# Kernel optimization log

Measured on AMD Instinct MI355X. Metric: run time of the kernel, lower is better.

The kernel has to match this reference:

```python
import jax, jax.numpy as jnp
import numpy as np

STRIDE = 1
MAX_STRIDE = 250  # 25 * 10 default


def setup_inputs() -> dict:
    key = jax.random.key(0)
    k1, k2 = jax.random.split(key)
    T = 1_000_000
    prediction = jax.random.normal(k1, (T,), dtype=jnp.float32)
    ground_truth = jax.random.normal(k2, (T,), dtype=jnp.float32)
    return {"prediction": prediction, "ground_truth": ground_truth}


def reference(prediction, ground_truth):
    T = prediction.shape[0]
    lags = jnp.arange(0, MAX_STRIDE, STRIDE)
    idx = jnp.arange(T)

    # ground-truth statistics are lag-independent
    mean_gt = jnp.mean(ground_truth)
    var_gt = jnp.var(ground_truth, ddof=1)  # torch.var is unbiased
    v_gt = ground_truth - mean_gt

    def ccc_at_lag(n):
        # shifted pred: n leading zeros followed by prediction[:-n]
        src = idx - n
        pred = jnp.where(src >= 0, prediction[jnp.clip(src, 0)], 0.0)
        mean_pred = jnp.mean(pred)
        var_pred = jnp.var(pred, ddof=1)
        cov = jnp.mean((pred - mean_pred) * v_gt)  # population covariance
        denom = var_gt + var_pred + (mean_gt - mean_pred) ** 2
        return 2.0 * cov / denom

    cccs = jax.vmap(ccc_at_lag)(lags)  # [n_lags]
    return 1.0 - jnp.mean(cccs)
```

## Files before the change

### kernel.cpp

```cpp
#include <hip/hip_runtime.h>
#include <hip/hip_bf16.h>


#define TC 4096
#define NTHR 512
#define NLAG 256
#define NUSED 250
#define NREP 16
#define GT4 (TC / 4 + 66)
#define STATREP_OFF (NREP * NLAG)
#define COUNTER_OFF (STATREP_OFF + NREP * 16)

__device__ __forceinline__ float4 ld_gt_sw(const float* s_gt, int i4) {
    int s = i4 ^ ((i4 >> 3) & 7);
    return *(const float4*)&s_gt[4 * s];
}

__device__ __forceinline__ float ld_atomic(const float* p) {
    return __hip_atomic_load(p, __ATOMIC_RELAXED, __HIP_MEMORY_SCOPE_AGENT);
}

__global__ __launch_bounds__(NTHR) void ccc_fused(const float* __restrict__ pred,
                                                  const float* __restrict__ gt,
                                                  float* __restrict__ ws,
                                                  float* __restrict__ out,
                                                  int T, int nch) {
    __shared__ __align__(16) float s_pred[TC];
    __shared__ __align__(16) float s_gt[GT4 * 4];
    __shared__ __align__(16) float s_acc[16][NLAG];
    __shared__ float s_red[8][4];
    __shared__ float s_stats[4];
    __shared__ float s_sp64[64];
    __shared__ unsigned s_last;

    const int tid = threadIdx.x;
    const int c = blockIdx.x;
    const int j0 = c * TC;

    float sp = 0.f, qp = 0.f, sg = 0.f, qg = 0.f;
    #pragma unroll 2
    for (int i4 = tid; i4 < TC / 4; i4 += NTHR) {
        int g = j0 + 4 * i4;
        float4 v = make_float4(0.f, 0.f, 0.f, 0.f);
        if (g + 3 < T) v = *(const float4*)&pred[g];
        *(float4*)&s_pred[4 * i4] = v;
        sp += v.x + v.y + v.z + v.w;
        qp += v.x * v.x + v.y * v.y + v.z * v.z + v.w * v.w;
    }
    #pragma unroll 2
    for (int i4 = tid; i4 < GT4; i4 += NTHR) {
        int g = j0 + 4 * i4;
        float4 v = make_float4(0.f, 0.f, 0.f, 0.f);
        if (g + 3 < T) v = *(const float4*)&gt[g];
        int s = i4 ^ ((i4 >> 3) & 7);
        *(float4*)&s_gt[4 * s] = v;
        if (i4 < TC / 4) {
            sg += v.x + v.y + v.z + v.w;
            qg += v.x * v.x + v.y * v.y + v.z * v.z + v.w * v.w;
        }
    }
    __syncthreads();

    const int sub = tid >> 5;
    const int l = tid & 31;
    int gi = sub * 64 + 2 * l;
    const int pi0 = sub * 64;

    float w[12];
    {
        float4 a = ld_gt_sw(s_gt, gi);
        float4 b = ld_gt_sw(s_gt, gi + 1);
        float4 d = ld_gt_sw(s_gt, gi + 2);
        w[0] = a.x; w[1] = a.y; w[2] = a.z; w[3] = a.w;
        w[4] = b.x; w[5] = b.y; w[6] = b.z; w[7] = b.w;
        w[8] = d.x; w[9] = d.y; w[10] = d.z; w[11] = d.w;
    }
    float acc[8] = {0.f, 0.f, 0.f, 0.f, 0.f, 0.f, 0.f, 0.f};

    #pragma unroll 8
    for (int it = 0; it < 64; ++it) {
        float4 nw = ld_gt_sw(s_gt, gi + 3 + it);
        float4 p = *(const float4*)&s_pred[4 * (pi0 + it)];
        #pragma unroll
        for (int k = 0; k < 8; ++k) {
            acc[k] = fmaf(p.x, w[k], acc[k]);
            acc[k] = fmaf(p.y, w[k + 1], acc[k]);
            acc[k] = fmaf(p.z, w[k + 2], acc[k]);
            acc[k] = fmaf(p.w, w[k + 3], acc[k]);
        }
        #pragma unroll
        for (int i = 0; i < 8; ++i) w[i] = w[i + 4];
        w[8] = nw.x; w[9] = nw.y; w[10] = nw.z; w[11] = nw.w;
    }

    const int wv = tid >> 6, ln = tid & 63;
    #pragma unroll
    for (int off = 32; off > 0; off >>= 1) {
        sp += __shfl_down(sp, off, 64);
        qp += __shfl_down(qp, off, 64);
        sg += __shfl_down(sg, off, 64);
        qg += __shfl_down(qg, off, 64);
    }
    if (ln == 0) { s_red[wv][0] = sp; s_red[wv][1] = qp; s_red[wv][2] = sg; s_red[wv][3] = qg; }

    #pragma unroll
    for (int k = 0; k < 8; ++k) s_acc[sub][8 * l + k] = acc[k];
    __syncthreads();

    const int rep = c & (NREP - 1);
    if (tid < NLAG) {
        float lagsum = 0.f;
        #pragma unroll
        for (int s = 0; s < 16; ++s) lagsum += s_acc[s][tid];
        atomicAdd(&ws[rep * NLAG + tid], lagsum);
    }
    if (tid < 4) {
        float v = 0.f;
        #pragma unroll
        for (int w8 = 0; w8 < 8; ++w8) v += s_red[w8][tid];
        atomicAdd(&ws[STATREP_OFF + rep * 16 + tid], v);
    }

    __syncthreads();
    if (tid == 0) {
        unsigned* cnt = (unsigned*)(ws + COUNTER_OFF);
        unsigned old = __hip_atomic_fetch_add(cnt, 1u, __ATOMIC_RELAXED,
                                              __HIP_MEMORY_SCOPE_AGENT);
        unsigned want_poison = 0xAAAAAAAAu + (unsigned)(nch - 1);
        unsigned want_zero = (unsigned)(nch - 1);
        s_last = (old == want_poison || old == want_zero) ? 1u : 0u;
    }
    __syncthreads();
    if (!s_last) return;

    {
        const int lag = tid & 255, h = tid >> 8;
        float a = 0.f;
        #pragma unroll
        for (int r = 8 * h; r < 8 * h + 8; ++r) a += ld_atomic(&ws[r * NLAG + lag]);
        s_acc[h][lag] = a;
    }
    if (tid < 64) s_sp64[tid] = ld_atomic(&ws[STATREP_OFF + (tid >> 2) * 16 + (tid & 3)]);
    if (tid < NLAG) {
        float x = pred[T - NLAG + tid];
        s_pred[tid] = x;
        s_acc[2][tid] = x;
        s_acc[4][tid] = x * x;
    }
    __syncthreads();

    if (tid < 4) {
        float s = 0.f;
        #pragma unroll
        for (int r = 0; r < 16; ++r) s += s_sp64[4 * r + tid];
        s_stats[tid] = s;
    }

    float *sa = s_acc[2], *sb = s_acc[3], *qa = s_acc[4], *qb = s_acc[5];
    for (int d = 1; d < NLAG; d <<= 1) {
        __syncthreads();
        if (tid < NLAG) {
            sb[tid] = sa[tid] + ((tid + d < NLAG) ? sa[tid + d] : 0.f);
            qb[tid] = qa[tid] + ((tid + d < NLAG) ? qa[tid + d] : 0.f);
        }
        float* tmp = sa; sa = sb; sb = tmp;
        tmp = qa; qa = qb; qb = tmp;
    }
    __syncthreads();

    if (tid < NLAG) {
        float lagC = s_acc[0][tid] + s_acc[1][tid];
        float v = 0.f;
        if (tid < NUSED) {
            const float Tf = (float)T;
            float sum_pred = s_stats[0], sumsq_pred = s_stats[1];
            float sum_gt = s_stats[2], sumsq_gt = s_stats[3];
            float mean_gt = sum_gt / Tf;
            float var_gt = (sumsq_gt - sum_gt * sum_gt / Tf) / (Tf - 1.f);
            float tail_s = (tid == 0) ? 0.f : sa[NLAG - tid];
            float tail_q = (tid == 0) ? 0.f : qa[NLAG - tid];
            float S = sum_pred - tail_s;
            float Q = sumsq_pred - tail_q;
            float mean_p = S / Tf;
            float var_p = (Q - S * S / Tf) / (Tf - 1.f);
            float cov = (lagC - mean_gt * S) / Tf;
            float dm = mean_gt - mean_p;
            v = 2.f * cov / (var_gt + var_p + dm * dm);
        }
        s_acc[6][tid] = v;
    }
    __syncthreads();
    for (int s = 128; s > 0; s >>= 1) {
        if (tid < s) s_acc[6][tid] += s_acc[6][tid + s];
        __syncthreads();
    }
    if (tid == 0) out[0] = 1.f - s_acc[6][0] / (float)NUSED;
}

extern "C" void kernel_launch(void* const* d_in, const int* in_sizes, int n_in,
                              void* d_out, int out_size, void* d_ws, size_t ws_size,
                              hipStream_t stream) {
    const float* pred = (const float*)d_in[0];
    const float* gt   = (const float*)d_in[1];
    float* out = (float*)d_out;
    float* ws  = (float*)d_ws;
    const int T = in_sizes[0];
    const int nch = (T + TC - 1) / TC;

    ccc_fused<<<nch, NTHR, 0, stream>>>(pred, gt, ws, out, T, nch);
}
```

Measured before the change: 71.24 us.

## Use packed float2 FMAs for lag correlation and hoist bounds checks

```diff
diff --git a/kernel.cpp b/kernel.cpp
--- a/kernel.cpp
+++ b/kernel.cpp
@@ -10,6 +10,8 @@
 #define GT4 (TC / 4 + 66)
 #define STATREP_OFF (NREP * NLAG)
 #define COUNTER_OFF (STATREP_OFF + NREP * 16)
+
+typedef float f2 __attribute__((ext_vector_type(2)));
 
 __device__ __forceinline__ float4 ld_gt_sw(const float* s_gt, int i4) {
     int s = i4 ^ ((i4 >> 3) & 7);
@@ -38,25 +40,45 @@
     const int j0 = c * TC;
 
     float sp = 0.f, qp = 0.f, sg = 0.f, qg = 0.f;
-    #pragma unroll 2
-    for (int i4 = tid; i4 < TC / 4; i4 += NTHR) {
-        int g = j0 + 4 * i4;
-        float4 v = make_float4(0.f, 0.f, 0.f, 0.f);
-        if (g + 3 < T) v = *(const float4*)&pred[g];
-        *(float4*)&s_pred[4 * i4] = v;
-        sp += v.x + v.y + v.z + v.w;
-        qp += v.x * v.x + v.y * v.y + v.z * v.z + v.w * v.w;
-    }
-    #pragma unroll 2
-    for (int i4 = tid; i4 < GT4; i4 += NTHR) {
-        int g = j0 + 4 * i4;
-        float4 v = make_float4(0.f, 0.f, 0.f, 0.f);
-        if (g + 3 < T) v = *(const float4*)&gt[g];
-        int s = i4 ^ ((i4 >> 3) & 7);
-        *(float4*)&s_gt[4 * s] = v;
-        if (i4 < TC / 4) {
-            sg += v.x + v.y + v.z + v.w;
-            qg += v.x * v.x + v.y * v.y + v.z * v.z + v.w * v.w;
+    if (j0 + 4 * GT4 <= T) {
+        #pragma unroll 2
+        for (int i4 = tid; i4 < TC / 4; i4 += NTHR) {
+            float4 v = *(const float4*)&pred[j0 + 4 * i4];
+            *(float4*)&s_pred[4 * i4] = v;
+            sp += v.x + v.y + v.z + v.w;
+            qp += v.x * v.x + v.y * v.y + v.z * v.z + v.w * v.w;
+        }
+        #pragma unroll 2
+        for (int i4 = tid; i4 < GT4; i4 += NTHR) {
+            float4 v = *(const float4*)&gt[j0 + 4 * i4];
+            int s = i4 ^ ((i4 >> 3) & 7);
+            *(float4*)&s_gt[4 * s] = v;
+            if (i4 < TC / 4) {
+                sg += v.x + v.y + v.z + v.w;
+                qg += v.x * v.x + v.y * v.y + v.z * v.z + v.w * v.w;
+            }
+        }
+    } else {
+        #pragma unroll 2
+        for (int i4 = tid; i4 < TC / 4; i4 += NTHR) {
+            int g = j0 + 4 * i4;
+            float4 v = make_float4(0.f, 0.f, 0.f, 0.f);
+            if (g + 3 < T) v = *(const float4*)&pred[g];
+            *(float4*)&s_pred[4 * i4] = v;
+            sp += v.x + v.y + v.z + v.w;
+            qp += v.x * v.x + v.y * v.y + v.z * v.z + v.w * v.w;
+        }
+        #pragma unroll 2
+        for (int i4 = tid; i4 < GT4; i4 += NTHR) {
+            int g = j0 + 4 * i4;
+            float4 v = make_float4(0.f, 0.f, 0.f, 0.f);
+            if (g + 3 < T) v = *(const float4*)&gt[g];
+            int s = i4 ^ ((i4 >> 3) & 7);
+            *(float4*)&s_gt[4 * s] = v;
+            if (i4 < TC / 4) {
+                sg += v.x + v.y + v.z + v.w;
+                qg += v.x * v.x + v.y * v.y + v.z * v.z + v.w * v.w;
+            }
         }
     }
     __syncthreads();
@@ -66,31 +88,39 @@
     int gi = sub * 64 + 2 * l;
     const int pi0 = sub * 64;
 
-    float w[12];
+    f2 E[6], O[5];
     {
         float4 a = ld_gt_sw(s_gt, gi);
         float4 b = ld_gt_sw(s_gt, gi + 1);
         float4 d = ld_gt_sw(s_gt, gi + 2);
-        w[0] = a.x; w[1] = a.y; w[2] = a.z; w[3] = a.w;
-        w[4] = b.x; w[5] = b.y; w[6] = b.z; w[7] = b.w;
-        w[8] = d.x; w[9] = d.y; w[10] = d.z; w[11] = d.w;
-    }
-    float acc[8] = {0.f, 0.f, 0.f, 0.f, 0.f, 0.f, 0.f, 0.f};
+        E[0] = f2{a.x, a.y}; E[1] = f2{a.z, a.w};
+        E[2] = f2{b.x, b.y}; E[3] = f2{b.z, b.w};
+        E[4] = f2{d.x, d.y}; E[5] = f2{d.z, d.w};
+        O[0] = f2{a.y, a.z}; O[1] = f2{a.w, b.x};
+        O[2] = f2{b.y, b.z}; O[3] = f2{b.w, d.x};
+        O[4] = f2{d.y, d.z};
+    }
+    f2 acc2[8];
+    #pragma unroll
+    for (int k = 0; k < 8; ++k) acc2[k] = f2{0.f, 0.f};
 
     #pragma unroll 8
     for (int it = 0; it < 64; ++it) {
         float4 nw = ld_gt_sw(s_gt, gi + 3 + it);
         float4 p = *(const float4*)&s_pred[4 * (pi0 + it)];
-        #pragma unroll
-        for (int k = 0; k < 8; ++k) {
-            acc[k] = fmaf(p.x, w[k], acc[k]);
-            acc[k] = fmaf(p.y, w[k + 1], acc[k]);
-            acc[k] = fmaf(p.z, w[k + 2], acc[k]);
-            acc[k] = fmaf(p.w, w[k + 3], acc[k]);
-        }
-        #pragma unroll
-        for (int i = 0; i < 8; ++i) w[i] = w[i + 4];
-        w[8] = nw.x; w[9] = nw.y; w[10] = nw.z; w[11] = nw.w;
+        f2 pA = f2{p.x, p.y}, pB = f2{p.z, p.w};
+        #pragma unroll
+        for (int m = 0; m < 4; ++m) {
+            acc2[2 * m]     = __builtin_elementwise_fma(pA, E[m],     acc2[2 * m]);
+            acc2[2 * m]     = __builtin_elementwise_fma(pB, E[m + 1], acc2[2 * m]);
+            acc2[2 * m + 1] = __builtin_elementwise_fma(pA, O[m],     acc2[2 * m + 1]);
+            acc2[2 * m + 1] = __builtin_elementwise_fma(pB, O[m + 1], acc2[2 * m + 1]);
+        }
+        float w11 = E[5].y;
+        E[0] = E[2]; E[1] = E[3]; E[2] = E[4]; E[3] = E[5];
+        E[4] = f2{nw.x, nw.y}; E[5] = f2{nw.z, nw.w};
+        O[0] = O[2]; O[1] = O[3]; O[2] = O[4];
+        O[3] = f2{w11, nw.x}; O[4] = f2{nw.y, nw.z};
     }
 
     const int wv = tid >> 6, ln = tid & 63;
@@ -104,7 +134,7 @@
     if (ln == 0) { s_red[wv][0] = sp; s_red[wv][1] = qp; s_red[wv][2] = sg; s_red[wv][3] = qg; }
 
     #pragma unroll
-    for (int k = 0; k < 8; ++k) s_acc[sub][8 * l + k] = acc[k];
+    for (int k = 0; k < 8; ++k) s_acc[sub][8 * l + k] = acc2[k].x + acc2[k].y;
     __syncthreads();
 
     const int rep = c & (NREP - 1);
```

Result: no change. 70.90 us (-0.5%).
